# Kernel optimization log

Measured on AMD Instinct MI355X. Metric: run time of the kernel, lower is better.

The kernel has to match this reference:

```python
import jax, jax.numpy as jnp
import numpy as np

PHI = 0.1  # fraction of pruned weights randomized per inference


def setup_inputs() -> dict:
    key = jax.random.key(0)
    k1, k2, k3 = jax.random.split(key, 3)
    d_out, d_in, batch = 8192, 8192, 256
    W = jax.random.normal(k1, (d_out, d_in), jnp.float32) * 0.02
    prune = jax.random.uniform(k2, (d_out, d_in)) < 0.9
    W = jnp.where(prune, 0.0, W)
    mask = (W == 0.0)  # _register_masks: pruned positions
    x = jax.random.normal(k3, (batch, d_in), jnp.float32)
    return {"x": x, "W": W, "mask": mask}


def reference(x, W, mask):
    # --- _apply_random_flip (vectorized) ---
    n_pruned = int(np.asarray(jnp.sum(mask)))          # concrete mask -> static count
    n_flip = max(1, int(PHI * n_pruned))
    keep = ~mask
    n_keep = jnp.sum(keep).astype(W.dtype)
    wk = jnp.where(keep, W, 0.0)
    mean = jnp.sum(wk) / n_keep
    # torch .std() is unbiased (n-1 denominator)
    var = jnp.sum(jnp.where(keep, (W - mean) ** 2, 0.0)) / (n_keep - 1.0)
    std = jnp.sqrt(var)
    key = jax.random.key(42)
    ks, kv = jax.random.split(key)
    # uniform random permutation of pruned indices -> top_k of random scores
    scores = jnp.where(mask.ravel(), jax.random.uniform(ks, (W.size,)), -1.0)
    _, flip_idx = jax.lax.top_k(scores, n_flip)        # [n_flip] flat indices into W
    vals = jax.random.normal(kv, (n_flip,), W.dtype) * std * 0.1
    W_flipped = W.ravel().at[flip_idx].set(vals).reshape(W.shape)
    # --- base_model forward (Linear, no bias) ---
    out = x @ W_flipped.T                               # [batch, d_out]
    # --- _restore_masks: zero flipped weights again (no effect on out) ---
    _ = jnp.where(mask, 0.0, W_flipped)
    return out
```

## Files before the change

### kernel.cpp

```cpp
#include <hip/hip_runtime.h>

typedef unsigned int u32;
typedef unsigned long long u64;
typedef unsigned short u16;

#define NTOT   67108864u
#define T0P    7399424u
#define PBASE  14452u
#define NSUP   1932u
#define NWSEG  4096u
#define WCAP   2176u
#define RCAP   4352u
#define KSPLIT 8

struct Scalars {
  double sumW;
  double sumW2;
  u64 npruned;
  u64 nflip;
  float stdf;
  float pad;
};

#define OFF_COLSUM 0ull
#define OFF_ALLOC  8192ull
#define OFF_SBASE  16384ull
#define OFF_SC     24576ull
#define OFF_SEGCNT 24704ull
#define OFF_BHIST  41216ull
#define OFF_BDEST  2138368ull
#define OFF_XBF    4235520ull
#define OFF_SEGS   8429824ull
#define OFF_ROUTED 44081408ull
#define OFF_WBF    81846400ull
#define WS_NEED_WBF 216064128ull
#define ROUTED_CAP 8912896u
#define OFF_OUTP   OFF_SEGS

__host__ __device__ inline void tf2x32(u32 k0, u32 k1, u32 x0, u32 x1, u32& y0, u32& y1) {
  u32 ks2 = k0 ^ k1 ^ 0x1BD11BDAu;
  x0 += k0; x1 += k1;
#define TFR(r) { x0 += x1; x1 = (x1 << (r)) | (x1 >> (32 - (r))); x1 ^= x0; }
  TFR(13) TFR(15) TFR(26) TFR(6)  x0 += k1;  x1 += ks2 + 1u;
  TFR(17) TFR(29) TFR(16) TFR(24) x0 += ks2; x1 += k0 + 2u;
  TFR(13) TFR(15) TFR(26) TFR(6)  x0 += k0;  x1 += k1 + 3u;
  TFR(17) TFR(29) TFR(16) TFR(24) x0 += k1;  x1 += ks2 + 4u;
  TFR(13) TFR(15) TFR(26) TFR(6)  x0 += ks2; x1 += k0 + 5u;
#undef TFR
  y0 = x0; y1 = x1;
}

__device__ inline u32 jax_bits32(u32 k0, u32 k1, u32 i) {
  u32 y0, y1; tf2x32(k0, k1, 0u, i, y0, y1);
  return y0 ^ y1;
}

__device__ inline u16 f2bf(float f) {
  union { float f; u32 u; } c; c.f = f;
  u32 r = ((c.u >> 16) & 1u) + 0x7FFFu;
  return (u16)((c.u + r) >> 16);
}

__device__ inline float erfinv32(float x) {
  float w = -log1pf(-x * x);
  float p;
  if (w < 5.0f) {
    w -= 2.5f;
    p = 2.81022636e-08f;
    p = fmaf(p, w, 3.43273939e-07f);
    p = fmaf(p, w, -3.5233877e-06f);
    p = fmaf(p, w, -4.39150654e-06f);
    p = fmaf(p, w, 0.00021858087f);
    p = fmaf(p, w, -0.00125372503f);
    p = fmaf(p, w, -0.00417768164f);
    p = fmaf(p, w, 0.246640727f);
    p = fmaf(p, w, 1.50140941f);
  } else {
    w = sqrtf(w) - 3.0f;
    p = -0.000200214257f;
    p = fmaf(p, w, 0.000100950558f);
    p = fmaf(p, w, 0.00134934322f);
    p = fmaf(p, w, -0.00367342844f);
    p = fmaf(p, w, 0.00573950773f);
    p = fmaf(p, w, -0.0076224613f);
    p = fmaf(p, w, 0.00943887047f);
    p = fmaf(p, w, 1.00167406f);
    p = fmaf(p, w, 2.83297682f);
  }
  return p * x;
}

__global__ __launch_bounds__(256) void k_pass1(const float* __restrict__ W, Scalars* sc,
                                               u32* segcnt, u32* segs, u32 uk0, u32 uk1) {
  u32 t = threadIdx.x;
  u32 gid = blockIdx.x * 256 + t;
  u32 lane = t & 63;
  u32 wid = gid >> 6;
  u32* wseg = segs + (u64)wid * WCAP;
  u32 wbase = 0;
  double s = 0.0, s2 = 0.0; u32 cnt = 0;
  const u32 stride4 = 1024u * 256u * 4u;
  for (u32 b4 = gid * 4; b4 < NTOT; b4 += stride4) {
    float4 w4 = *(const float4*)(W + b4);
    u32 sb0 = jax_bits32(uk0, uk1, b4 + 0) >> 9;
    u32 sb1 = jax_bits32(uk0, uk1, b4 + 1) >> 9;
    u32 sb2 = jax_bits32(uk0, uk1, b4 + 2) >> 9;
    u32 sb3 = jax_bits32(uk0, uk1, b4 + 3) >> 9;
    float we[4] = {w4.x, w4.y, w4.z, w4.w};
    u32 sbv[4] = {sb0, sb1, sb2, sb3};
    u32 cand[4]; u32 nc = 0;
#pragma unroll
    for (int e = 0; e < 4; e++) {
      float w = we[e];
      s  += (double)w;
      s2 += (double)w * (double)w;
      bool pr = (w == 0.0f);
      cnt += pr ? 1u : 0u;
      if (pr && sbv[e] >= T0P) { cand[nc] = b4 + e; nc++; }
    }
    u32 inc = nc;
#pragma unroll
    for (int o = 1; o < 64; o <<= 1) { u32 v = (u32)__shfl_up((int)inc, o); if (lane >= (u32)o) inc += v; }
    u32 tot = (u32)__shfl((int)inc, 63);
    u32 pos = wbase + inc - nc;
    for (u32 k2 = 0; k2 < nc; k2++)
      if (pos + k2 < WCAP) wseg[pos + k2] = cand[k2];
    wbase += tot;
  }
  for (int o = 32; o > 0; o >>= 1) {
    s += __shfl_down(s, o); s2 += __shfl_down(s2, o); cnt += __shfl_down(cnt, o);
  }
  if (lane == 0) {
    atomicAdd(&sc->sumW, s);
    atomicAdd(&sc->sumW2, s2);
    atomicAdd(&sc->npruned, (u64)cnt);
    segcnt[wid] = (wbase > WCAP) ? WCAP : wbase;
  }
}

__global__ __launch_bounds__(256) void k_wconv(const float* __restrict__ W,
                                               u16* __restrict__ wbf) {
  u32 i = blockIdx.x * 256 + threadIdx.x;
  const u32 stride = 4096u * 256u;
  for (u32 g = i; g < NTOT / 8; g += stride) {
    const float4* p = (const float4*)(W + (u64)g * 8);
    float4 a = p[0], b = p[1];
    uint4 o;
    o.x = (u32)f2bf(a.x) | ((u32)f2bf(a.y) << 16);
    o.y = (u32)f2bf(a.z) | ((u32)f2bf(a.w) << 16);
    o.z = (u32)f2bf(b.x) | ((u32)f2bf(b.y) << 16);
    o.w = (u32)f2bf(b.z) | ((u32)f2bf(b.w) << 16);
    *(uint4*)(wbf + (u64)g * 8) = o;
  }
}

__global__ __launch_bounds__(256) void k_route_a(const u32* __restrict__ segs,
                                                 const u32* __restrict__ segcnt,
                                                 u32* bhist, u32 uk0, u32 uk1) {
  __shared__ u32 lhist[2048];
  u32 t = threadIdx.x;
  for (u32 j = t; j < 2048; j += 256) lhist[j] = 0;
  __syncthreads();
#pragma unroll 1
  for (int sg = 0; sg < 16; sg++) {
    u32 wid = blockIdx.x * 16 + sg;
    u32 n = segcnt[wid]; if (n > WCAP) n = WCAP;
    const u32* sp = segs + (u64)wid * WCAP;
    for (u32 i = t; i < n; i += 256) {
      u32 sup = (jax_bits32(uk0, uk1, sp[i]) >> 18) - PBASE;
      atomicAdd(&lhist[sup], 1u);
    }
  }
  __syncthreads();
  for (u32 j = t; j < 2048; j += 256) bhist[blockIdx.x * 2048 + j] = lhist[j];
}

__global__ __launch_bounds__(256) void k_colscan(const u32* __restrict__ bhist,
                                                 u32* bdest, u32* colsum) {
  __shared__ u32 wtmp[4];
  u32 s = blockIdx.x, t = threadIdx.x, lane = t & 63, wv = t >> 6;
  u32 v = bhist[t * 2048 + s];
  u32 inc = v;
#pragma unroll
  for (int o = 1; o < 64; o <<= 1) { u32 x = (u32)__shfl_up((int)inc, o); if (lane >= (u32)o) inc += x; }
  if (lane == 63) wtmp[wv] = inc;
  __syncthreads();
  u32 woff = 0;
  for (u32 w = 0; w < wv; w++) woff += wtmp[w];
  bdest[t * 2048 + s] = woff + inc - v;
  if (t == 255) colsum[s] = woff + inc;
}

__global__ __launch_bounds__(256) void k_scan(const u32* __restrict__ colsum, Scalars* sc,
                                              u32* alloc, u32* sbase) {
  __shared__ u32 h[2048];
  __shared__ u32 wtmp[4];
  u32 t = threadIdx.x, lane = t & 63, wv = t >> 6;
  for (u32 j = t; j < 2048; j += 256) h[j] = colsum[j];
  __syncthreads();
  {
    u32 a[8]; u32 s8 = 0;
#pragma unroll
    for (int k = 0; k < 8; k++) { a[k] = h[t * 8 + k]; s8 += a[k]; }
    u32 inc = s8;
#pragma unroll
    for (int o = 1; o < 64; o <<= 1) { u32 v = (u32)__shfl_up((int)inc, o); if (lane >= (u32)o) inc += v; }
    if (lane == 63) wtmp[wv] = inc;
    __syncthreads();
    u32 woff = 0; for (u32 w = 0; w < wv; w++) woff += wtmp[w];
    u32 base = woff + inc - s8;
#pragma unroll
    for (int k = 0; k < 8; k++) { alloc[t * 8 + k] = base; base += a[k]; }
    __syncthreads();
  }
  {
    u32 a[8]; u32 s8 = 0;
#pragma unroll
    for (int k = 0; k < 8; k++) { a[k] = h[2047 - (t * 8 + k)]; s8 += a[k]; }
    u32 inc = s8;
#pragma unroll
    for (int o = 1; o < 64; o <<= 1) { u32 v = (u32)__shfl_up((int)inc, o); if (lane >= (u32)o) inc += v; }
    if (lane == 63) wtmp[wv] = inc;
    __syncthreads();
    u32 woff = 0; for (u32 w = 0; w < wv; w++) woff += wtmp[w];
    u32 base = woff + inc - s8;
#pragma unroll
    for (int k = 0; k < 8; k++) { sbase[2047 - (t * 8 + k)] = base; base += a[k]; }
  }
  if (t == 0) {
    double nk = (double)NTOT - (double)sc->npruned;
    double mean = sc->sumW / nk;
    double var = (sc->sumW2 - 2.0 * mean * sc->sumW + nk * mean * mean) / (nk - 1.0);
    sc->stdf = (float)sqrt(var);
    u64 nfi = (u64)(0.1 * (double)sc->npruned);
    if (nfi < 1) nfi = 1;
    sc->nflip = nfi;
  }
}

__global__ __launch_bounds__(256) void k_route_b(const u32* __restrict__ segs,
                                                 const u32* __restrict__ segcnt,
                                                 const u32* __restrict__ alloc,
                                                 const u32* __restrict__ bdest,
                                                 u32* routed, u32 uk0, u32 uk1) {
  __shared__ u32 lcur[2048];
  u32 t = threadIdx.x;
  for (u32 j = t; j < 2048; j += 256) lcur[j] = alloc[j] + bdest[blockIdx.x * 2048 + j];
  __syncthreads();
#pragma unroll 1
  for (int sg = 0; sg < 16; sg++) {
    u32 wid = blockIdx.x * 16 + sg;
    u32 n = segcnt[wid]; if (n > WCAP) n = WCAP;
    const u32* sp = segs + (u64)wid * WCAP;
    for (u32 i = t; i < n; i += 256) {
      u32 idx = sp[i];
      u32 sup = (jax_bits32(uk0, uk1, idx) >> 18) - PBASE;
      u32 pos = atomicAdd(&lcur[sup], 1u);
      if (pos < ROUTED_CAP) routed[pos] = idx;
    }
  }
}

__device__ inline void suf512(const u32* cnt, u32* suf, u32* wtmp) {
  u32 t = threadIdx.x, lane = t & 63, wv = t >> 6;
  u32 a0 = cnt[511 - t * 2], a1 = cnt[510 - t * 2];
  u32 s = a0 + a1;
  u32 inc = s;
#pragma unroll
  for (int o = 1; o < 64; o <<= 1) { u32 v = (u32)__shfl_up((int)inc, o); if (lane >= (u32)o) inc += v; }
  if (lane == 63) wtmp[wv] = inc;
  __syncthreads();
  u32 woff = 0;
  for (u32 w = 0; w < wv; w++) woff += wtmp[w];
  u32 base = woff + inc - s;
  suf[511 - t * 2] = base;
  suf[510 - t * 2] = base + a0;
  __syncthreads();
}

template<int WBF>
__global__ __launch_bounds__(256) void k_rank(float* __restrict__ W,
                                              u16* __restrict__ wbf,
                                              const u32* __restrict__ colsum,
                                              const u32* __restrict__ alloc,
                                              const u32* __restrict__ sbase,
                                              const u32* __restrict__ routed,
                                              const Scalars* __restrict__ sc,
                                              u32 uk0, u32 uk1, u32 vk0, u32 vk1) {
  u32 p = blockIdx.x;
  u32 n = colsum[p]; if (n == 0) return;
  if (n > RCAP) n = RCAP;
  u64 nflip = sc->nflip;
  u32 rbase = sbase[p];
  if ((u64)rbase >= nflip) return;
  __shared__ u32 sIdx[RCAP];
  __shared__ u16 sFine[RCAP];
  __shared__ u32 pIdx[RCAP];
  __shared__ u32 hist[512], gbase[512], cur[512], wtmp[4];
  u32 t = threadIdx.x;
  for (u32 j = t; j < 512; j += 256) hist[j] = 0;
  __syncthreads();
  const u32* src = routed + alloc[p];
  for (u32 i = t; i < n; i += 256) {
    u32 idx = src[i];
    u32 f = (jax_bits32(uk0, uk1, idx) >> 9) & 511u;
    sIdx[i] = idx;
    sFine[i] = (u16)f;
    atomicAdd(&hist[f], 1u);
  }
  __syncthreads();
  suf512(hist, gbase, wtmp);
  for (u32 j = t; j < 512; j += 256) cur[j] = gbase[j];
  __syncthreads();
  for (u32 i = t; i < n; i += 256) {
    u32 pos = atomicAdd(&cur[sFine[i]], 1u);
    pIdx[pos] = sIdx[i];
  }
  __syncthreads();
  float stdf = sc->stdf;
  for (u32 i = t; i < n; i += 256) {
    u32 f = sFine[i];
    u32 g0 = gbase[f], g1 = g0 + hist[f];
    u32 v = sIdx[i];
    u32 ord = 0;
    for (u32 q = g0; q < g1; q++) ord += (pIdx[q] < v) ? 1u : 0u;
    u64 rank = (u64)rbase + g0 + ord;
    if (rank >= nflip) continue;
    u32 bits = jax_bits32(vk0, vk1, (u32)rank);
    union { u32 u; float fl; } cv; cv.u = 0x3F800000u | (bits >> 9);
    float fu = cv.fl - 1.0f;
    const float lo = -0.99999994f;
    float u2 = fmaxf(lo, fu * 2.0f + lo);
    float nrm = 1.41421354f * erfinv32(u2);
    float val = (nrm * stdf) * 0.1f;
    if (WBF) wbf[v] = f2bf(val);
    else     W[v] = val;
  }
}

__global__ __launch_bounds__(256) void k_xconv(const float* __restrict__ x, u16* __restrict__ xbf) {
  u32 i = blockIdx.x * blockDim.x + threadIdx.x;
  float4 v = ((const float4*)x)[i];
  ushort4 o; o.x = f2bf(v.x); o.y = f2bf(v.y); o.z = f2bf(v.z); o.w = f2bf(v.w);
  ((ushort4*)xbf)[i] = o;
}

typedef __bf16 bf16x8 __attribute__((ext_vector_type(8)));
typedef float f32x4 __attribute__((ext_vector_type(4)));

__global__ __launch_bounds__(256, 3) void k_gemm2(const u16* __restrict__ xbf,
                                                  const u16* __restrict__ wbf,
                                                  float* __restrict__ outp) {
  __shared__ u16 As[128 * 64];
  __shared__ u16 Bs[128 * 64];
  u32 tid = threadIdx.x;
  u32 lane = tid & 63, wv = tid >> 6;
  u32 l8 = lane & 7;
  u32 lr = lane >> 3;
  u32 nrow = blockIdx.x * 128;
  u32 mrow = blockIdx.y * 128;
  u32 kbase = blockIdx.z * (8192u / KSPLIT);
  u32 wm = wv >> 1, wn = wv & 1;
  u32 r = lane & 15, q = lane >> 4;
  f32x4 acc[4][4];
#pragma unroll
  for (int i = 0; i < 4; i++)
#pragma unroll
    for (int j = 0; j < 4; j++) acc[i][j] = (f32x4){0.f, 0.f, 0.f, 0.f};

  for (u32 kb = kbase; kb < kbase + (8192u / KSPLIT); kb += 64u) {
#pragma unroll
    for (int j = 0; j < 4; j++) {
      u32 g = wv * 4 + (u32)j;
      u32 row = g * 8 + lr;
      u32 sc = ((l8 ^ (row & 7u)) * 8u);
      const u16* ga = xbf + (u64)(mrow + row) * 8192 + kb + sc;
      __builtin_amdgcn_global_load_lds((const u32*)ga, (u32*)&As[g * 512u], 16, 0, 0);
      const u16* gb = wbf + (u64)(nrow + row) * 8192 + kb + sc;
      __builtin_amdgcn_global_load_lds((const u32*)gb, (u32*)&Bs[g * 512u], 16, 0, 0);
    }
    __syncthreads();
#pragma unroll
    for (int ks = 0; ks < 2; ks++) {
      bf16x8 a[4], b[4];
      u32 ch = (u32)(ks * 4) + q;
#pragma unroll
      for (int mt = 0; mt < 4; mt++) {
        u32 row = wm * 64 + (u32)mt * 16 + r;
        a[mt] = *(bf16x8*)&As[row * 64 + ((ch ^ (r & 7u)) * 8u)];
      }
#pragma unroll
      for (int nt = 0; nt < 4; nt++) {
        u32 row = wn * 64 + (u32)nt * 16 + r;
        b[nt] = *(bf16x8*)&Bs[row * 64 + ((ch ^ (r & 7u)) * 8u)];
      }
#pragma unroll
      for (int mt = 0; mt < 4; mt++)
#pragma unroll
        for (int nt = 0; nt < 4; nt++)
          acc[mt][nt] = __builtin_amdgcn_mfma_f32_16x16x32_bf16(a[mt], b[nt], acc[mt][nt], 0, 0, 0);
    }
    __syncthreads();
  }
  float* op = outp + (u64)blockIdx.z * 2097152u;
  u32 quad = lane >> 4, col = lane & 15;
#pragma unroll
  for (int mt = 0; mt < 4; mt++)
#pragma unroll
    for (int nt = 0; nt < 4; nt++) {
      u32 n = nrow + wn * 64 + (u32)nt * 16 + col;
#pragma unroll
      for (int rg = 0; rg < 4; rg++) {
        u32 m = mrow + wm * 64 + (u32)mt * 16 + quad * 4 + (u32)rg;
        op[(u64)m * 8192 + n] = acc[mt][nt][rg];
      }
    }
}

__global__ __launch_bounds__(256) void k_redout(const float* __restrict__ part,
                                                float* __restrict__ out) {
  u32 i = blockIdx.x * 256 + threadIdx.x;
  float4 s = ((const float4*)part)[i];
#pragma unroll
  for (int k = 1; k < KSPLIT; k++) {
    float4 v = ((const float4*)(part + (u64)k * 2097152u))[i];
    s.x += v.x; s.y += v.y; s.z += v.z; s.w += v.w;
  }
  ((float4*)out)[i] = s;
}

__global__ __launch_bounds__(256, 2) void k_gemm_fb(const u16* __restrict__ xbf,
                                                    const float* __restrict__ W,
                                                    float* __restrict__ out) {
  __shared__ u16 xs[256 * 72];
  __shared__ u16 wsm[64 * 72];
  u32 tid = threadIdx.x;
  u32 lane = tid & 63, wv = tid >> 6;
  u32 nt0 = blockIdx.x * 64;
  u32 kbase = blockIdx.y * 2048u;
  f32x4 acc[4][4];
#pragma unroll
  for (int i = 0; i < 4; i++)
#pragma unroll
    for (int j = 0; j < 4; j++) acc[i][j] = (f32x4){0.f, 0.f, 0.f, 0.f};
  for (u32 kb = kbase; kb < kbase + 2048u; kb += 64u) {
#pragma unroll
    for (int r8 = 0; r8 < 8; r8++) {
      u32 row = r8 * 32 + (tid >> 3);
      u32 kseg = (tid & 7) * 8;
      uint4 v = *(const uint4*)(xbf + (u64)row * 8192 + kb + kseg);
      *(uint4*)&xs[row * 72 + kseg] = v;
    }
#pragma unroll
    for (int rr = 0; rr < 4; rr++) {
      u32 f4 = rr * 256 + tid;
      u32 row = f4 >> 4;
      u32 kc = (f4 & 15) * 4;
      float4 v = *(const float4*)(W + (u64)(nt0 + row) * 8192 + kb + kc);
      ushort4 o; o.x = f2bf(v.x); o.y = f2bf(v.y); o.z = f2bf(v.z); o.w = f2bf(v.w);
      *(ushort4*)&wsm[row * 72 + kc] = o;
    }
    __syncthreads();
#pragma unroll
    for (int ks = 0; ks < 2; ks++) {
      bf16x8 a[4], b[4];
      u32 koff = ks * 32 + (lane >> 4) * 8;
      u32 rsel = lane & 15;
#pragma unroll
      for (int mt = 0; mt < 4; mt++) a[mt] = *(bf16x8*)&xs[(wv * 64 + mt * 16 + rsel) * 72 + koff];
#pragma unroll
      for (int nt = 0; nt < 4; nt++) b[nt] = *(bf16x8*)&wsm[(nt * 16 + rsel) * 72 + koff];
#pragma unroll
      for (int mt = 0; mt < 4; mt++)
#pragma unroll
        for (int nt = 0; nt < 4; nt++)
          acc[mt][nt] = __builtin_amdgcn_mfma_f32_16x16x32_bf16(a[mt], b[nt], acc[mt][nt], 0, 0, 0);
    }
    __syncthreads();
  }
  u32 quad = lane >> 4, col = lane & 15;
#pragma unroll
  for (int mt = 0; mt < 4; mt++)
#pragma unroll
    for (int nt = 0; nt < 4; nt++) {
      u32 n = nt0 + nt * 16 + col;
#pragma unroll
      for (int rg = 0; rg < 4; rg++) {
        u32 m = wv * 64 + mt * 16 + quad * 4 + rg;
        atomicAdd(&out[(u64)m * 8192 + n], acc[mt][nt][rg]);
      }
    }
}

extern "C" void kernel_launch(void* const* d_in, const int* in_sizes, int n_in,
                              void* d_out, int out_size, void* d_ws, size_t ws_size,
                              hipStream_t stream) {
  const float* x; float* W;
  if (in_sizes[0] == 2097152) { x = (const float*)d_in[0]; W = (float*)d_in[1]; }
  else                        { x = (const float*)d_in[1]; W = (float*)d_in[0]; }
  float* out = (float*)d_out;
  char* ws = (char*)d_ws;

  u32* colsum = (u32*)(ws + OFF_COLSUM);
  u32* alloc  = (u32*)(ws + OFF_ALLOC);
  u32* sbase  = (u32*)(ws + OFF_SBASE);
  Scalars* sc = (Scalars*)(ws + OFF_SC);
  u32* segcnt = (u32*)(ws + OFF_SEGCNT);
  u32* bhist  = (u32*)(ws + OFF_BHIST);
  u32* bdest  = (u32*)(ws + OFF_BDEST);
  u16* xbf    = (u16*)(ws + OFF_XBF);
  u32* segs   = (u32*)(ws + OFF_SEGS);
  u32* routed = (u32*)(ws + OFF_ROUTED);
  u16* wbf    = (u16*)(ws + OFF_WBF);
  float* outp = (float*)(ws + OFF_OUTP);

  bool usewbf = (ws_size >= (size_t)WS_NEED_WBF);

  u32 a0, a1, b0, b1;
  tf2x32(0u, 42u, 0u, 0u, a0, a1);
  tf2x32(0u, 42u, 0u, 1u, b0, b1);

  hipMemsetAsync(sc, 0, sizeof(Scalars), stream);

  k_xconv<<<2048, 256, 0, stream>>>(x, xbf);
  k_pass1<<<1024, 256, 0, stream>>>(W, sc, segcnt, segs, a0, a1);
  if (usewbf) k_wconv<<<4096, 256, 0, stream>>>(W, wbf);
  k_route_a<<<256, 256, 0, stream>>>(segs, segcnt, bhist, a0, a1);
  k_colscan<<<2048, 256, 0, stream>>>(bhist, bdest, colsum);
  k_scan<<<1, 256, 0, stream>>>(colsum, sc, alloc, sbase);
  k_route_b<<<256, 256, 0, stream>>>(segs, segcnt, alloc, bdest, routed, a0, a1);
  if (usewbf) {
    k_rank<1><<<NSUP, 256, 0, stream>>>(W, wbf, colsum, alloc, sbase, routed, sc, a0, a1, b0, b1);
    dim3 g(64, 2, KSPLIT);
    k_gemm2<<<g, 256, 0, stream>>>(xbf, wbf, outp);
    k_redout<<<2048, 256, 0, stream>>>(outp, out);
  } else {
    k_rank<0><<<NSUP, 256, 0, stream>>>(W, wbf, colsum, alloc, sbase, routed, sc, a0, a1, b0, b1);
    hipMemsetAsync(out, 0, (size_t)out_size * 4, stream);
    dim3 g(128, 4);
    k_gemm_fb<<<g, 256, 0, stream>>>(xbf, W, out);
  }
}
```

Baseline: 1.025 ms.

## Fuse W bf16 conversion into pass1 launch and double routing block count

Merges the fp32-to-bf16 weight conversion into the statistics/candidate pass as extra blocks of the same launch, so the ALU-heavy RNG pass and the bandwidth-bound conversion can run concurrently instead of back to back. The routing kernels now use 512 blocks with 8 segments each instead of 256 with 16, which raises parallelism. The column scan is changed to sum two histogram rows per thread to match, and the workspace offsets are shifted to fit the larger histogram. This costs more histogram traffic and a smaller routed-buffer capacity.

```diff
diff --git a/kernel.cpp b/kernel.cpp
--- a/kernel.cpp
+++ b/kernel.cpp
@@ -12,6 +12,8 @@
 #define WCAP   2176u
 #define RCAP   4352u
 #define KSPLIT 8
+#define RBLK   512u
+#define SEGPB  8
 
 struct Scalars {
   double sumW;
@@ -28,13 +30,13 @@
 #define OFF_SC     24576ull
 #define OFF_SEGCNT 24704ull
 #define OFF_BHIST  41216ull
-#define OFF_BDEST  2138368ull
-#define OFF_XBF    4235520ull
-#define OFF_SEGS   8429824ull
-#define OFF_ROUTED 44081408ull
+#define OFF_BDEST  4235520ull
+#define OFF_XBF    8429824ull
+#define OFF_SEGS   12624128ull
+#define OFF_ROUTED 48275712ull
 #define OFF_WBF    81846400ull
 #define WS_NEED_WBF 216064128ull
-#define ROUTED_CAP 8912896u
+#define ROUTED_CAP 8388608u
 #define OFF_OUTP   OFF_SEGS
 
 __host__ __device__ inline void tf2x32(u32 k0, u32 k1, u32 x0, u32 x1, u32& y0, u32& y1) {
@@ -90,67 +92,69 @@
   return p * x;
 }
 
-__global__ __launch_bounds__(256) void k_pass1(const float* __restrict__ W, Scalars* sc,
-                                               u32* segcnt, u32* segs, u32 uk0, u32 uk1) {
+__global__ __launch_bounds__(256) void k_pass1w(const float* __restrict__ W,
+                                                u16* __restrict__ wbf, Scalars* sc,
+                                                u32* segcnt, u32* segs,
+                                                u32 uk0, u32 uk1) {
   u32 t = threadIdx.x;
-  u32 gid = blockIdx.x * 256 + t;
-  u32 lane = t & 63;
-  u32 wid = gid >> 6;
-  u32* wseg = segs + (u64)wid * WCAP;
-  u32 wbase = 0;
-  double s = 0.0, s2 = 0.0; u32 cnt = 0;
-  const u32 stride4 = 1024u * 256u * 4u;
-  for (u32 b4 = gid * 4; b4 < NTOT; b4 += stride4) {
-    float4 w4 = *(const float4*)(W + b4);
-    u32 sb0 = jax_bits32(uk0, uk1, b4 + 0) >> 9;
-    u32 sb1 = jax_bits32(uk0, uk1, b4 + 1) >> 9;
-    u32 sb2 = jax_bits32(uk0, uk1, b4 + 2) >> 9;
-    u32 sb3 = jax_bits32(uk0, uk1, b4 + 3) >> 9;
-    float we[4] = {w4.x, w4.y, w4.z, w4.w};
-    u32 sbv[4] = {sb0, sb1, sb2, sb3};
-    u32 cand[4]; u32 nc = 0;
-#pragma unroll
-    for (int e = 0; e < 4; e++) {
-      float w = we[e];
-      s  += (double)w;
-      s2 += (double)w * (double)w;
-      bool pr = (w == 0.0f);
-      cnt += pr ? 1u : 0u;
-      if (pr && sbv[e] >= T0P) { cand[nc] = b4 + e; nc++; }
-    }
-    u32 inc = nc;
-#pragma unroll
-    for (int o = 1; o < 64; o <<= 1) { u32 v = (u32)__shfl_up((int)inc, o); if (lane >= (u32)o) inc += v; }
-    u32 tot = (u32)__shfl((int)inc, 63);
-    u32 pos = wbase + inc - nc;
-    for (u32 k2 = 0; k2 < nc; k2++)
-      if (pos + k2 < WCAP) wseg[pos + k2] = cand[k2];
-    wbase += tot;
-  }
-  for (int o = 32; o > 0; o >>= 1) {
-    s += __shfl_down(s, o); s2 += __shfl_down(s2, o); cnt += __shfl_down(cnt, o);
-  }
-  if (lane == 0) {
-    atomicAdd(&sc->sumW, s);
-    atomicAdd(&sc->sumW2, s2);
-    atomicAdd(&sc->npruned, (u64)cnt);
-    segcnt[wid] = (wbase > WCAP) ? WCAP : wbase;
-  }
-}
-
-__global__ __launch_bounds__(256) void k_wconv(const float* __restrict__ W,
-                                               u16* __restrict__ wbf) {
-  u32 i = blockIdx.x * 256 + threadIdx.x;
-  const u32 stride = 4096u * 256u;
-  for (u32 g = i; g < NTOT / 8; g += stride) {
-    const float4* p = (const float4*)(W + (u64)g * 8);
-    float4 a = p[0], b = p[1];
-    uint4 o;
-    o.x = (u32)f2bf(a.x) | ((u32)f2bf(a.y) << 16);
-    o.y = (u32)f2bf(a.z) | ((u32)f2bf(a.w) << 16);
-    o.z = (u32)f2bf(b.x) | ((u32)f2bf(b.y) << 16);
-    o.w = (u32)f2bf(b.z) | ((u32)f2bf(b.w) << 16);
-    *(uint4*)(wbf + (u64)g * 8) = o;
+  u32 bid = blockIdx.x;
+  if (bid < 1024u) {
+    u32 gid = bid * 256 + t;
+    u32 lane = t & 63;
+    u32 wid = gid >> 6;
+    u32* wseg = segs + (u64)wid * WCAP;
+    u32 wbase = 0;
+    double s = 0.0, s2 = 0.0; u32 cnt = 0;
+    const u32 stride4 = 1024u * 256u * 4u;
+    for (u32 b4 = gid * 4; b4 < NTOT; b4 += stride4) {
+      float4 w4 = *(const float4*)(W + b4);
+      u32 sb0 = jax_bits32(uk0, uk1, b4 + 0) >> 9;
+      u32 sb1 = jax_bits32(uk0, uk1, b4 + 1) >> 9;
+      u32 sb2 = jax_bits32(uk0, uk1, b4 + 2) >> 9;
+      u32 sb3 = jax_bits32(uk0, uk1, b4 + 3) >> 9;
+      float we[4] = {w4.x, w4.y, w4.z, w4.w};
+      u32 sbv[4] = {sb0, sb1, sb2, sb3};
+      u32 cand[4]; u32 nc = 0;
+#pragma unroll
+      for (int e = 0; e < 4; e++) {
+        float w = we[e];
+        s  += (double)w;
+        s2 += (double)w * (double)w;
+        bool pr = (w == 0.0f);
+        cnt += pr ? 1u : 0u;
+        if (pr && sbv[e] >= T0P) { cand[nc] = b4 + e; nc++; }
+      }
+      u32 inc = nc;
+#pragma unroll
+      for (int o = 1; o < 64; o <<= 1) { u32 v = (u32)__shfl_up((int)inc, o); if (lane >= (u32)o) inc += v; }
+      u32 tot = (u32)__shfl((int)inc, 63);
+      u32 pos = wbase + inc - nc;
+      for (u32 k2 = 0; k2 < nc; k2++)
+        if (pos + k2 < WCAP) wseg[pos + k2] = cand[k2];
+      wbase += tot;
+    }
+    for (int o = 32; o > 0; o >>= 1) {
+      s += __shfl_down(s, o); s2 += __shfl_down(s2, o); cnt += __shfl_down(cnt, o);
+    }
+    if (lane == 0) {
+      atomicAdd(&sc->sumW, s);
+      atomicAdd(&sc->sumW2, s2);
+      atomicAdd(&sc->npruned, (u64)cnt);
+      segcnt[wid] = (wbase > WCAP) ? WCAP : wbase;
+    }
+  } else {
+    u32 i0 = (bid - 1024u) * 256 + t;
+    const u32 stride = 1024u * 256u;
+    for (u32 g = i0; g < NTOT / 8; g += stride) {
+      const float4* p = (const float4*)(W + (u64)g * 8);
+      float4 a = p[0], b = p[1];
+      uint4 o;
+      o.x = (u32)f2bf(a.x) | ((u32)f2bf(a.y) << 16);
+      o.y = (u32)f2bf(a.z) | ((u32)f2bf(a.w) << 16);
+      o.z = (u32)f2bf(b.x) | ((u32)f2bf(b.y) << 16);
+      o.w = (u32)f2bf(b.z) | ((u32)f2bf(b.w) << 16);
+      *(uint4*)(wbf + (u64)g * 8) = o;
+    }
   }
 }
 
@@ -162,8 +166,8 @@
   for (u32 j = t; j < 2048; j += 256) lhist[j] = 0;
   __syncthreads();
 #pragma unroll 1
-  for (int sg = 0; sg < 16; sg++) {
-    u32 wid = blockIdx.x * 16 + sg;
+  for (int sg = 0; sg < SEGPB; sg++) {
+    u32 wid = blockIdx.x * SEGPB + sg;
     u32 n = segcnt[wid]; if (n > WCAP) n = WCAP;
     const u32* sp = segs + (u64)wid * WCAP;
     for (u32 i = t; i < n; i += 256) {
@@ -179,15 +183,19 @@
                                                  u32* bdest, u32* colsum) {
   __shared__ u32 wtmp[4];
   u32 s = blockIdx.x, t = threadIdx.x, lane = t & 63, wv = t >> 6;
-  u32 v = bhist[t * 2048 + s];
-  u32 inc = v;
+  u32 v0 = bhist[(t * 2 + 0) * 2048 + s];
+  u32 v1 = bhist[(t * 2 + 1) * 2048 + s];
+  u32 pr = v0 + v1;
+  u32 inc = pr;
 #pragma unroll
   for (int o = 1; o < 64; o <<= 1) { u32 x = (u32)__shfl_up((int)inc, o); if (lane >= (u32)o) inc += x; }
   if (lane == 63) wtmp[wv] = inc;
   __syncthreads();
   u32 woff = 0;
   for (u32 w = 0; w < wv; w++) woff += wtmp[w];
-  bdest[t * 2048 + s] = woff + inc - v;
+  u32 base = woff + inc - pr;
+  bdest[(t * 2 + 0) * 2048 + s] = base;
+  bdest[(t * 2 + 1) * 2048 + s] = base + v0;
   if (t == 255) colsum[s] = woff + inc;
 }
 
@@ -248,8 +256,8 @@
   for (u32 j = t; j < 2048; j += 256) lcur[j] = alloc[j] + bdest[blockIdx.x * 2048 + j];
   __syncthreads();
 #pragma unroll 1
-  for (int sg = 0; sg < 16; sg++) {
-    u32 wid = blockIdx.x * 16 + sg;
+  for (int sg = 0; sg < SEGPB; sg++) {
+    u32 wid = blockIdx.x * SEGPB + sg;
     u32 n = segcnt[wid]; if (n > WCAP) n = WCAP;
     const u32* sp = segs + (u64)wid * WCAP;
     for (u32 i = t; i < n; i += 256) {
@@ -523,12 +531,11 @@
   hipMemsetAsync(sc, 0, sizeof(Scalars), stream);
 
   k_xconv<<<2048, 256, 0, stream>>>(x, xbf);
-  k_pass1<<<1024, 256, 0, stream>>>(W, sc, segcnt, segs, a0, a1);
-  if (usewbf) k_wconv<<<4096, 256, 0, stream>>>(W, wbf);
-  k_route_a<<<256, 256, 0, stream>>>(segs, segcnt, bhist, a0, a1);
+  k_pass1w<<<usewbf ? 2048 : 1024, 256, 0, stream>>>(W, wbf, sc, segcnt, segs, a0, a1);
+  k_route_a<<<RBLK, 256, 0, stream>>>(segs, segcnt, bhist, a0, a1);
   k_colscan<<<2048, 256, 0, stream>>>(bhist, bdest, colsum);
   k_scan<<<1, 256, 0, stream>>>(colsum, sc, alloc, sbase);
-  k_route_b<<<256, 256, 0, stream>>>(segs, segcnt, alloc, bdest, routed, a0, a1);
+  k_route_b<<<RBLK, 256, 0, stream>>>(segs, segcnt, alloc, bdest, routed, a0, a1);
   if (usewbf) {
     k_rank<1><<<NSUP, 256, 0, stream>>>(W, wbf, colsum, alloc, sbase, routed, sc, a0, a1, b0, b1);
     dim3 g(64, 2, KSPLIT);
```

Measured after the change: 1.009 ms. No clear change (-1.6%).
